# Kernel tuning notes

Hardware: AMD Instinct MI355X
Metric: run time of the kernel (lower is better)

## Reference

```python
import jax, jax.numpy as jnp
import numpy as np

T, B, IN, H = 256, 128, 512, 1024


def setup_inputs() -> dict:
    key = jax.random.key(0)
    ks = jax.random.split(key, 13)
    s = 1.0 / float(np.sqrt(H))  # torch LSTMCell init: U(-1/sqrt(H), 1/sqrt(H))
    u = lambda k, shp: jax.random.uniform(k, shp, jnp.float32, -s, s)
    return {
        "x": jax.random.normal(ks[0], (T, B, IN), jnp.float32),
        "h0_fwd": jax.random.normal(ks[1], (B, H), jnp.float32),
        "c0_fwd": jax.random.normal(ks[2], (B, H), jnp.float32),
        "h0_rev": jax.random.normal(ks[3], (B, H), jnp.float32),
        "c0_rev": jax.random.normal(ks[4], (B, H), jnp.float32),
        "W_ih_f": u(ks[5], (4 * H, IN)),
        "W_hh_f": u(ks[6], (4 * H, H)),
        "b_ih_f": u(ks[7], (4 * H,)),
        "b_hh_f": u(ks[8], (4 * H,)),
        "W_ih_r": u(ks[9], (4 * H, IN)),
        "W_hh_r": u(ks[10], (4 * H, H)),
        "b_ih_r": u(ks[11], (4 * H,)),
        "b_hh_r": u(ks[12], (4 * H,)),
    }


def _lstm(x, h0, c0, Wih, Whh, bih, bhh, reverse):
    # Precompute the input projection for all timesteps in one big GEMM.
    xp = jnp.einsum('tbi,gi->tbg', x, Wih) + bih + bhh  # [T, B, 4H]

    def step(carry, xg):
        h, c = carry
        gates = xg + h @ Whh.T  # [B, 4H]
        i, f, g, o = jnp.split(gates, 4, axis=-1)  # torch gate order: i, f, g, o
        c = jax.nn.sigmoid(f) * c + jax.nn.sigmoid(i) * jnp.tanh(g)
        h = jax.nn.sigmoid(o) * jnp.tanh(c)
        return (h, c), h

    # reverse=True scans backward in time but emits outputs in original order,
    # exactly matching ReverseLSTMLayer's reverse-process-then-reverse-outputs.
    (h, c), ys = jax.lax.scan(step, (h0, c0), xp, reverse=reverse)
    return ys, h, c


def reference(x, h0_fwd, c0_fwd, h0_rev, c0_rev,
              W_ih_f, W_hh_f, b_ih_f, b_hh_f,
              W_ih_r, W_hh_r, b_ih_r, b_hh_r):
    yf, hf, cf = _lstm(x, h0_fwd, c0_fwd, W_ih_f, W_hh_f, b_ih_f, b_hh_f, False)
    yr, hr, cr = _lstm(x, h0_rev, c0_rev, W_ih_r, W_hh_r, b_ih_r, b_hh_r, True)
    out = jnp.concatenate([yf, yr], axis=-1)  # [T, B, 2H]
    # Faithful to the original's `hidden, cell = output_states` quirk:
    # `hidden` is the forward direction's (h, c) pair stacked,
    # `cell` is the reverse direction's (h, c) pair stacked.
    hidden = jnp.stack([hf, cf])  # [2, B, H]
    cell = jnp.stack([hr, cr])    # [2, B, H]
    return out, (hidden, cell)
```

## Files before the change

### kernel.cpp

```cpp
#include <hip/hip_runtime.h>
#include <hip/hip_bf16.h>

typedef unsigned short u16;
typedef __attribute__((ext_vector_type(8))) short bf16x8;
typedef __attribute__((ext_vector_type(8))) u16   u16x8;
typedef __attribute__((ext_vector_type(4))) float f32x4;

#define T_STEPS 256
#define BATCH   128
#define INDIM   512
#define HDIM    1024
#define GDIM    4096
#define KTOT    1536

#define OFF_XBF   ((size_t)0)
#define XBF_BYTES ((size_t)T_STEPS * BATCH * INDIM * 2)
#define OFF_BM    (OFF_XBF + XBF_BYTES)
#define BM_BYTES  ((size_t)2 * GDIM * KTOT * 2)
#define OFF_BIAS  (OFF_BM + BM_BYTES)
#define BIAS_BYTES ((size_t)2 * GDIM * 4)
#define OFF_CNT   (OFF_BIAS + BIAS_BYTES)
#define OFF_ROLL  (OFF_CNT + 8192)
#define ROLL_BYTES ((size_t)(T_STEPS + 1) * 2 * BATCH * HDIM * 2)
#define WS_NEED   (OFF_ROLL + ROLL_BYTES)

__device__ __forceinline__ u16 f2b(float f) {
  __hip_bfloat16 h = __float2bfloat16(f);
  return *reinterpret_cast<u16*>(&h);
}

__device__ __forceinline__ void glds16(const void* g, void* l) {
  __builtin_amdgcn_global_load_lds(
      (const __attribute__((address_space(1))) unsigned int*)g,
      (__attribute__((address_space(3))) unsigned int*)l, 16, 0, 0);
}

__global__ void k_cast_x(const float* __restrict__ x, u16* __restrict__ xs) {
  int i = blockIdx.x * 256 + threadIdx.x;
  int t   = i >> 13;
  int r13 = i & 8191;
  int row = r13 >> 6;
  int c0  = (r13 & 63) * 8;
  int q = row >> 5, rloc = row & 31;
  int mi = rloc >> 4, ar = rloc & 15;
  int kq = c0 >> 7, kr = c0 & 127;
  int ks = kr >> 5, h4 = (kr & 31) >> 3;
  int lane = h4 * 16 + ar;
  const float* src = x + ((size_t)t * BATCH + row) * INDIM + c0;
  f32x4 a = *reinterpret_cast<const f32x4*>(src);
  f32x4 b = *reinterpret_cast<const f32x4*>(src + 4);
  u16x8 u;
  u[0] = f2b(a[0]); u[1] = f2b(a[1]); u[2] = f2b(a[2]); u[3] = f2b(a[3]);
  u[4] = f2b(b[0]); u[5] = f2b(b[1]); u[6] = f2b(b[2]); u[7] = f2b(b[3]);
  size_t dst = ((((((size_t)t * 4 + q) * 4 + kq) * 4 + ks) * 2 + mi) * 64 + lane) * 8;
  *reinterpret_cast<u16x8*>(xs + dst) = u;
}

__global__ void k_build_b(const float* __restrict__ Whh_f, const float* __restrict__ Wih_f,
                          const float* __restrict__ Whh_r, const float* __restrict__ Wih_r,
                          u16* __restrict__ Bm) {
  int blk = blockIdx.x;
  int dir = blk >> 5, jt = blk & 31;
  const float* Whh = dir ? Whh_r : Whh_f;
  const float* Wih = dir ? Wih_r : Wih_f;
  u16* dst = Bm + (size_t)blk * 128 * KTOT;
  for (int c = 0; c < 128; c++) {
    int G = (c >> 5) * HDIM + jt * 32 + (c & 31);
    for (int k = threadIdx.x; k < KTOT; k += 256) {
      float v = (k < HDIM) ? Whh[(size_t)G * HDIM + k] : Wih[(size_t)G * INDIM + (k - HDIM)];
      dst[c * KTOT + k] = f2b(v);
    }
  }
}

__global__ void k_init(const float* __restrict__ h0f, const float* __restrict__ h0r,
                       const float* __restrict__ bihf, const float* __restrict__ bhhf,
                       const float* __restrict__ bihr, const float* __restrict__ bhhr,
                       u16* __restrict__ hroll, float* __restrict__ bias,
                       unsigned* __restrict__ flags) {
  int i = blockIdx.x * 256 + threadIdx.x;
  if (i < 2 * BATCH * HDIM) {
    int dir = i / (BATCH * HDIM);
    int rem = i - dir * BATCH * HDIM;
    int r = rem / HDIM, c = rem - r * HDIM;
    const float* h0 = dir ? h0r : h0f;
    char* hb = (char*)hroll;
    *(u16*)(hb + ((size_t)dir * BATCH + r) * 2048 + ((2 * c) ^ ((r & 7) << 4))) =
        f2b(h0[rem]);
  }
  if (i < 2 * GDIM) {
    int dir = i / GDIM, g = i - dir * GDIM;
    bias[i] = dir ? (bihr[g] + bhhr[g]) : (bihf[g] + bhhf[g]);
  }
  if (i < 512) flags[i] = 0;
}

__global__ __launch_bounds__(512, 2) void k_lstm(
    const u16* __restrict__ xs, const u16* __restrict__ Bm,
    u16* __restrict__ hroll,
    const float* __restrict__ bias, unsigned* __restrict__ flags,
    const float* __restrict__ c0f, const float* __restrict__ c0r,
    float* __restrict__ out) {
  __shared__ float ldsf[34816];
  char* ldsc = reinterpret_cast<char*>(ldsf);
  float* ldsP = ldsf + 16384;

  __builtin_amdgcn_fence(__ATOMIC_ACQUIRE, "agent");

  const int wg   = blockIdx.x;
  const int grp  = wg & 7;
  const int dir  = grp >> 2, q = grp & 3;
  const int jt32 = wg >> 3;
  const int tid  = threadIdx.x;
  const int w = tid >> 6, lane = tid & 63;
  const int kq = w >> 1, nh = w & 1;
  const int h4 = lane >> 4, kk = h4 * 8;
  const int ar = lane & 15;

  const u16* bsrc = Bm + (size_t)(dir * 32 + jt32) * 128 * KTOT;
  bf16x8 bh[8][4], bx[4][4];
#pragma unroll
  for (int ks = 0; ks < 8; ks++)
#pragma unroll
    for (int ni = 0; ni < 4; ni++)
      bh[ks][ni] = *reinterpret_cast<const bf16x8*>(
          bsrc + (size_t)(nh * 64 + ni * 16 + ar) * KTOT + 256 * kq + 32 * ks + kk);
#pragma unroll
  for (int ks = 0; ks < 4; ks++)
#pragma unroll
    for (int ni = 0; ni < 4; ni++)
      bx[ks][ni] = *reinterpret_cast<const bf16x8*>(
          bsrc + (size_t)(nh * 64 + ni * 16 + ar) * KTOT + HDIM + 128 * kq + 32 * ks + kk);

  const int rrow = tid & 31;
  const int jl0  = 2 * (tid >> 5);
  const int row0 = q * 32 + rrow;
  const int jg0  = jt32 * 32 + jl0;
  const float* c0 = dir ? c0r : c0f;
  float2 cc = *reinterpret_cast<const float2*>(c0 + (size_t)row0 * HDIM + jg0);
  float cst0 = cc.x, cst1 = cc.y;
  const float2 b_i = *reinterpret_cast<const float2*>(bias + dir * GDIM + 0 * HDIM + jg0);
  const float2 b_f = *reinterpret_cast<const float2*>(bias + dir * GDIM + 1 * HDIM + jg0);
  const float2 b_g = *reinterpret_cast<const float2*>(bias + dir * GDIM + 2 * HDIM + jg0);
  const float2 b_o = *reinterpret_cast<const float2*>(bias + dir * GDIM + 3 * HDIM + jg0);

  const unsigned* fpA = flags + grp * 32 + (lane & 31);

#pragma unroll 1
  for (int s = 0; s < T_STEPS; s++) {
    const int t = dir ? (T_STEPS - 1 - s) : s;

    bf16x8 ax[4][2];
    {
      const u16* xb = xs + ((((size_t)t * 4 + q) * 4 + kq) * 4) * 2 * 512;
#pragma unroll
      for (int ks = 0; ks < 4; ks++)
#pragma unroll
        for (int mi = 0; mi < 2; mi++)
          ax[ks][mi] = *reinterpret_cast<const bf16x8*>(
              xb + ((size_t)(ks * 2 + mi) * 64 + lane) * 8);
    }

    if (s > 0) {
      while (true) {
        unsigned f = __hip_atomic_load(fpA, __ATOMIC_RELAXED, __HIP_MEMORY_SCOPE_AGENT);
        if (__all((int)(f >= (unsigned)s))) break;
        __builtin_amdgcn_s_sleep(1);
      }
      __builtin_amdgcn_sched_barrier(0);
    }

    {
      const char* hRd = (const char*)hroll + ((size_t)s * 2 + dir) * (BATCH * 2048)
                        + (size_t)q * 32 * 2048;
      unsigned off = (unsigned)tid * 16;
#pragma unroll
      for (int i = 0; i < 8; i++)
        glds16(hRd + off + i * 8192, ldsc + off + i * 8192);
    }
    __builtin_amdgcn_sched_barrier(0);

    f32x4 acc[2][4];
#pragma unroll
    for (int mi = 0; mi < 2; mi++)
#pragma unroll
      for (int ni = 0; ni < 4; ni++) acc[mi][ni] = f32x4{0.f, 0.f, 0.f, 0.f};
#pragma unroll
    for (int ks = 0; ks < 4; ks++)
#pragma unroll
      for (int mi = 0; mi < 2; mi++)
#pragma unroll
        for (int ni = 0; ni < 4; ni++)
          acc[mi][ni] = __builtin_amdgcn_mfma_f32_16x16x32_bf16(ax[ks][mi], bx[ks][ni], acc[mi][ni], 0, 0, 0);

    __syncthreads();

#pragma unroll
    for (int ks = 0; ks < 8; ks++) {
      bf16x8 af[2];
#pragma unroll
      for (int mi = 0; mi < 2; mi++) {
        unsigned row = 16 * mi + ar;
        unsigned cb = (256 * kq + 32 * ks + kk) * 2;
        af[mi] = *reinterpret_cast<const bf16x8*>(
            ldsc + row * 2048 + (cb ^ ((row & 7) << 4)));
      }
#pragma unroll
      for (int mi = 0; mi < 2; mi++)
#pragma unroll
        for (int ni = 0; ni < 4; ni++)
          acc[mi][ni] = __builtin_amdgcn_mfma_f32_16x16x32_bf16(af[mi], bh[ks][ni], acc[mi][ni], 0, 0, 0);
    }

    {
      float* pw = ldsP + kq * (128 * 36);
#pragma unroll
      for (int mi = 0; mi < 2; mi++)
#pragma unroll
        for (int ni = 0; ni < 4; ni++) {
          int col = nh * 64 + ni * 16 + ar;
          *reinterpret_cast<f32x4*>(pw + col * 36 + mi * 16 + h4 * 4) = acc[mi][ni];
        }
    }
    __syncthreads();

    float h0v, h1v;
    {
      float gi0 = b_i.x, gi1 = b_i.y, gf0 = b_f.x, gf1 = b_f.y;
      float gg0 = b_g.x, gg1 = b_g.y, go0 = b_o.x, go1 = b_o.y;
#pragma unroll
      for (int k4 = 0; k4 < 4; k4++) {
        const float* p = ldsP + k4 * (128 * 36);
        gi0 += p[(0 * 32 + jl0) * 36 + rrow]; gi1 += p[(0 * 32 + jl0 + 1) * 36 + rrow];
        gf0 += p[(1 * 32 + jl0) * 36 + rrow]; gf1 += p[(1 * 32 + jl0 + 1) * 36 + rrow];
        gg0 += p[(2 * 32 + jl0) * 36 + rrow]; gg1 += p[(2 * 32 + jl0 + 1) * 36 + rrow];
        go0 += p[(3 * 32 + jl0) * 36 + rrow]; go1 += p[(3 * 32 + jl0 + 1) * 36 + rrow];
      }
      float i0 = 1.f / (1.f + __expf(-gi0)), i1 = 1.f / (1.f + __expf(-gi1));
      float f0 = 1.f / (1.f + __expf(-gf0)), f1 = 1.f / (1.f + __expf(-gf1));
      float g0 = tanhf(gg0), g1 = tanhf(gg1);
      float o0 = 1.f / (1.f + __expf(-go0)), o1 = 1.f / (1.f + __expf(-go1));
      cst0 = f0 * cst0 + i0 * g0;
      cst1 = f1 * cst1 + i1 * g1;
      h0v = o0 * tanhf(cst0);
      h1v = o1 * tanhf(cst1);

      unsigned hp = (unsigned)f2b(h0v) | ((unsigned)f2b(h1v) << 16);
      char* hb = (char*)hroll + ((size_t)(s + 1) * 2 + dir) * (BATCH * 2048);
      __hip_atomic_store(
          (unsigned*)(hb + (size_t)row0 * 2048 + ((2 * jg0) ^ ((row0 & 7) << 4))),
          hp, __ATOMIC_RELAXED, __HIP_MEMORY_SCOPE_AGENT);
    }

    asm volatile("s_waitcnt vmcnt(0)" ::: "memory");
    __syncthreads();
    if (tid == 0)
      __hip_atomic_store(flags + grp * 32 + jt32, (unsigned)(s + 1),
                         __ATOMIC_RELAXED, __HIP_MEMORY_SCOPE_AGENT);

    {
      float2 yv; yv.x = h0v; yv.y = h1v;
      *reinterpret_cast<float2*>(out + ((size_t)t * BATCH + row0) * (2 * HDIM)
                                     + (size_t)dir * HDIM + jg0) = yv;
      if (s == T_STEPS - 1) {
        size_t hid = (size_t)T_STEPS * BATCH * 2 * HDIM;
        size_t base2 = hid + (size_t)dir * 2 * BATCH * HDIM;
        *reinterpret_cast<float2*>(out + base2 + (size_t)row0 * HDIM + jg0) = yv;
        float2 cv; cv.x = cst0; cv.y = cst1;
        *reinterpret_cast<float2*>(out + base2 + (size_t)BATCH * HDIM
                                       + (size_t)row0 * HDIM + jg0) = cv;
      }
    }
  }
}

extern "C" void kernel_launch(void* const* d_in, const int* in_sizes, int n_in,
                              void* d_out, int out_size, void* d_ws, size_t ws_size,
                              hipStream_t stream) {
  const float* x     = (const float*)d_in[0];
  const float* h0f   = (const float*)d_in[1];
  const float* c0f   = (const float*)d_in[2];
  const float* h0r   = (const float*)d_in[3];
  const float* c0r   = (const float*)d_in[4];
  const float* Wih_f = (const float*)d_in[5];
  const float* Whh_f = (const float*)d_in[6];
  const float* bih_f = (const float*)d_in[7];
  const float* bhh_f = (const float*)d_in[8];
  const float* Wih_r = (const float*)d_in[9];
  const float* Whh_r = (const float*)d_in[10];
  const float* bih_r = (const float*)d_in[11];
  const float* bhh_r = (const float*)d_in[12];
  float* out = (float*)d_out;
  char* ws = (char*)d_ws;

  if (ws_size < WS_NEED) return;

  u16* xsf        = (u16*)(ws + OFF_XBF);
  u16* Bm         = (u16*)(ws + OFF_BM);
  float* bias     = (float*)(ws + OFF_BIAS);
  unsigned* flags = (unsigned*)(ws + OFF_CNT);
  u16* hroll      = (u16*)(ws + OFF_ROLL);

  k_cast_x<<<8192, 256, 0, stream>>>(x, xsf);
  k_build_b<<<64, 256, 0, stream>>>(Whh_f, Wih_f, Whh_r, Wih_r, Bm);
  k_init<<<1024, 256, 0, stream>>>(h0f, h0r, bih_f, bhh_f, bih_r, bhh_r,
                                   hroll, bias, flags);
  k_lstm<<<256, 512, 0, stream>>>(xsf, Bm, hroll, bias, flags, c0f, c0r, out);
}
```

Before: 2.292 ms.

## Simplify x cast layout, reblock weights, alias LDS buffers, retune reduction padding

Several changes at once. The x cast becomes a plain row-major bf16 conversion and the LSTM kernel reads MFMA fragments directly with strided loads. The weight panel is rebuilt in 16-column blocks, and the LDS h buffer and partial-sum buffer now share one allocation, which needs an extra barrier. The partial-sum row pitch changes from 36 to 33, the gate thread mapping is swapped, and the h store scope drops to workgroup. The workgroup-scope store risks cross-workgroup visibility problems, and the strided x loads may be less coalesced.

```diff
diff --git a/kernel.cpp b/kernel.cpp
--- a/kernel.cpp
+++ b/kernel.cpp
@@ -35,37 +35,26 @@
       (__attribute__((address_space(3))) unsigned int*)l, 16, 0, 0);
 }
 
-__global__ void k_cast_x(const float* __restrict__ x, u16* __restrict__ xs) {
-  int i = blockIdx.x * 256 + threadIdx.x;
-  int t   = i >> 13;
-  int r13 = i & 8191;
-  int row = r13 >> 6;
-  int c0  = (r13 & 63) * 8;
-  int q = row >> 5, rloc = row & 31;
-  int mi = rloc >> 4, ar = rloc & 15;
-  int kq = c0 >> 7, kr = c0 & 127;
-  int ks = kr >> 5, h4 = (kr & 31) >> 3;
-  int lane = h4 * 16 + ar;
-  const float* src = x + ((size_t)t * BATCH + row) * INDIM + c0;
-  f32x4 a = *reinterpret_cast<const f32x4*>(src);
-  f32x4 b = *reinterpret_cast<const f32x4*>(src + 4);
+__global__ void k_cast_x(const float* __restrict__ x, u16* __restrict__ xb) {
+  size_t i = ((size_t)blockIdx.x * 256 + threadIdx.x) * 8;
+  f32x4 a = *reinterpret_cast<const f32x4*>(x + i);
+  f32x4 b = *reinterpret_cast<const f32x4*>(x + i + 4);
   u16x8 u;
   u[0] = f2b(a[0]); u[1] = f2b(a[1]); u[2] = f2b(a[2]); u[3] = f2b(a[3]);
   u[4] = f2b(b[0]); u[5] = f2b(b[1]); u[6] = f2b(b[2]); u[7] = f2b(b[3]);
-  size_t dst = ((((((size_t)t * 4 + q) * 4 + kq) * 4 + ks) * 2 + mi) * 64 + lane) * 8;
-  *reinterpret_cast<u16x8*>(xs + dst) = u;
+  *reinterpret_cast<u16x8*>(xb + i) = u;
 }
 
 __global__ void k_build_b(const float* __restrict__ Whh_f, const float* __restrict__ Wih_f,
                           const float* __restrict__ Whh_r, const float* __restrict__ Wih_r,
                           u16* __restrict__ Bm) {
   int blk = blockIdx.x;
-  int dir = blk >> 5, jt = blk & 31;
+  int dir = blk >> 6, jt = blk & 63;
   const float* Whh = dir ? Whh_r : Whh_f;
   const float* Wih = dir ? Wih_r : Wih_f;
-  u16* dst = Bm + (size_t)blk * 128 * KTOT;
-  for (int c = 0; c < 128; c++) {
-    int G = (c >> 5) * HDIM + jt * 32 + (c & 31);
+  u16* dst = Bm + (size_t)blk * 64 * KTOT;
+  for (int c = 0; c < 64; c++) {
+    int G = (c >> 4) * HDIM + jt * 16 + (c & 15);
     for (int k = threadIdx.x; k < KTOT; k += 256) {
       float v = (k < HDIM) ? Whh[(size_t)G * HDIM + k] : Wih[(size_t)G * INDIM + (k - HDIM)];
       dst[c * KTOT + k] = f2b(v);
@@ -96,44 +85,42 @@
 }
 
 __global__ __launch_bounds__(512, 2) void k_lstm(
-    const u16* __restrict__ xs, const u16* __restrict__ Bm,
+    const u16* __restrict__ xb, const u16* __restrict__ Bm,
     u16* __restrict__ hroll,
     const float* __restrict__ bias, unsigned* __restrict__ flags,
     const float* __restrict__ c0f, const float* __restrict__ c0r,
     float* __restrict__ out) {
-  __shared__ float ldsf[34816];
-  char* ldsc = reinterpret_cast<char*>(ldsf);
-  float* ldsP = ldsf + 16384;
+  __shared__ char ldsc[67584];
+  float* ldsP = reinterpret_cast<float*>(ldsc);
 
   __builtin_amdgcn_fence(__ATOMIC_ACQUIRE, "agent");
 
   const int wg   = blockIdx.x;
-  const int grp  = wg & 7;
-  const int dir  = grp >> 2, q = grp & 3;
+  const int xcd  = wg & 7;
+  const int dir  = xcd >> 2, q = xcd & 3;
   const int jt32 = wg >> 3;
+  const int grp  = dir * 4 + q;
   const int tid  = threadIdx.x;
   const int w = tid >> 6, lane = tid & 63;
   const int kq = w >> 1, nh = w & 1;
   const int h4 = lane >> 4, kk = h4 * 8;
   const int ar = lane & 15;
 
-  const u16* bsrc = Bm + (size_t)(dir * 32 + jt32) * 128 * KTOT;
   bf16x8 bh[8][4], bx[4][4];
 #pragma unroll
-  for (int ks = 0; ks < 8; ks++)
-#pragma unroll
-    for (int ni = 0; ni < 4; ni++)
-      bh[ks][ni] = *reinterpret_cast<const bf16x8*>(
-          bsrc + (size_t)(nh * 64 + ni * 16 + ar) * KTOT + 256 * kq + 32 * ks + kk);
-#pragma unroll
-  for (int ks = 0; ks < 4; ks++)
-#pragma unroll
-    for (int ni = 0; ni < 4; ni++)
-      bx[ks][ni] = *reinterpret_cast<const bf16x8*>(
-          bsrc + (size_t)(nh * 64 + ni * 16 + ar) * KTOT + HDIM + 128 * kq + 32 * ks + kk);
-
-  const int rrow = tid & 31;
-  const int jl0  = 2 * (tid >> 5);
+  for (int ni = 0; ni < 4; ni++) {
+    const u16* bp = Bm + (size_t)(dir * 64 + jt32 * 2 + (ni & 1)) * 64 * KTOT
+                  + (size_t)((nh * 2 + (ni >> 1)) * 16 + ar) * KTOT;
+#pragma unroll
+    for (int ks = 0; ks < 8; ks++)
+      bh[ks][ni] = *reinterpret_cast<const bf16x8*>(bp + 256 * kq + 32 * ks + kk);
+#pragma unroll
+    for (int ksx = 0; ksx < 4; ksx++)
+      bx[ksx][ni] = *reinterpret_cast<const bf16x8*>(bp + HDIM + 128 * kq + 32 * ksx + kk);
+  }
+
+  const int rrow = tid >> 4;
+  const int jl0  = 2 * (tid & 15);
   const int row0 = q * 32 + rrow;
   const int jg0  = jt32 * 32 + jl0;
   const float* c0 = dir ? c0r : c0f;
@@ -152,13 +139,13 @@
 
     bf16x8 ax[4][2];
     {
-      const u16* xb = xs + ((((size_t)t * 4 + q) * 4 + kq) * 4) * 2 * 512;
-#pragma unroll
-      for (int ks = 0; ks < 4; ks++)
+      const u16* xsrc = xb + ((size_t)t * BATCH + q * 32) * INDIM;
+#pragma unroll
+      for (int ksx = 0; ksx < 4; ksx++)
 #pragma unroll
         for (int mi = 0; mi < 2; mi++)
-          ax[ks][mi] = *reinterpret_cast<const bf16x8*>(
-              xb + ((size_t)(ks * 2 + mi) * 64 + lane) * 8);
+          ax[ksx][mi] = *reinterpret_cast<const bf16x8*>(
+              xsrc + (size_t)(16 * mi + ar) * INDIM + 128 * kq + 32 * ksx + kk);
     }
 
     if (s > 0) {
@@ -171,14 +158,13 @@
     }
 
     {
-      const char* hRd = (const char*)hroll + ((size_t)s * 2 + dir) * (BATCH * 2048)
-                        + (size_t)q * 32 * 2048;
+      const char* hRd = (const char*)hroll
+                      + ((size_t)(s * 2 + dir) * BATCH + q * 32) * 2048;
       unsigned off = (unsigned)tid * 16;
 #pragma unroll
       for (int i = 0; i < 8; i++)
         glds16(hRd + off + i * 8192, ldsc + off + i * 8192);
     }
-    __builtin_amdgcn_sched_barrier(0);
 
     f32x4 acc[2][4];
 #pragma unroll
@@ -186,12 +172,12 @@
 #pragma unroll
       for (int ni = 0; ni < 4; ni++) acc[mi][ni] = f32x4{0.f, 0.f, 0.f, 0.f};
 #pragma unroll
-    for (int ks = 0; ks < 4; ks++)
+    for (int ksx = 0; ksx < 4; ksx++)
 #pragma unroll
       for (int mi = 0; mi < 2; mi++)
 #pragma unroll
         for (int ni = 0; ni < 4; ni++)
-          acc[mi][ni] = __builtin_amdgcn_mfma_f32_16x16x32_bf16(ax[ks][mi], bx[ks][ni], acc[mi][ni], 0, 0, 0);
+          acc[mi][ni] = __builtin_amdgcn_mfma_f32_16x16x32_bf16(ax[ksx][mi], bx[ksx][ni], acc[mi][ni], 0, 0, 0);
 
     __syncthreads();
 
@@ -211,15 +197,16 @@
         for (int ni = 0; ni < 4; ni++)
           acc[mi][ni] = __builtin_amdgcn_mfma_f32_16x16x32_bf16(af[mi], bh[ks][ni], acc[mi][ni], 0, 0, 0);
     }
-
-    {
-      float* pw = ldsP + kq * (128 * 36);
+    __syncthreads();
+
+    {
+      float* pw = ldsP + kq * (128 * 33);
 #pragma unroll
       for (int mi = 0; mi < 2; mi++)
 #pragma unroll
         for (int ni = 0; ni < 4; ni++) {
           int col = nh * 64 + ni * 16 + ar;
-          *reinterpret_cast<f32x4*>(pw + col * 36 + mi * 16 + h4 * 4) = acc[mi][ni];
+          *reinterpret_cast<f32x4*>(pw + col * 33 + mi * 16 + h4 * 4) = acc[mi][ni];
         }
     }
     __syncthreads();
@@ -230,11 +217,11 @@
       float gg0 = b_g.x, gg1 = b_g.y, go0 = b_o.x, go1 = b_o.y;
 #pragma unroll
       for (int k4 = 0; k4 < 4; k4++) {
-        const float* p = ldsP + k4 * (128 * 36);
-        gi0 += p[(0 * 32 + jl0) * 36 + rrow]; gi1 += p[(0 * 32 + jl0 + 1) * 36 + rrow];
-        gf0 += p[(1 * 32 + jl0) * 36 + rrow]; gf1 += p[(1 * 32 + jl0 + 1) * 36 + rrow];
-        gg0 += p[(2 * 32 + jl0) * 36 + rrow]; gg1 += p[(2 * 32 + jl0 + 1) * 36 + rrow];
-        go0 += p[(3 * 32 + jl0) * 36 + rrow]; go1 += p[(3 * 32 + jl0 + 1) * 36 + rrow];
+        const float* p = ldsP + k4 * (128 * 33);
+        gi0 += p[(0 * 32 + jl0) * 33 + rrow]; gi1 += p[(0 * 32 + jl0 + 1) * 33 + rrow];
+        gf0 += p[(1 * 32 + jl0) * 33 + rrow]; gf1 += p[(1 * 32 + jl0 + 1) * 33 + rrow];
+        gg0 += p[(2 * 32 + jl0) * 33 + rrow]; gg1 += p[(2 * 32 + jl0 + 1) * 33 + rrow];
+        go0 += p[(3 * 32 + jl0) * 33 + rrow]; go1 += p[(3 * 32 + jl0 + 1) * 33 + rrow];
       }
       float i0 = 1.f / (1.f + __expf(-gi0)), i1 = 1.f / (1.f + __expf(-gi1));
       float f0 = 1.f / (1.f + __expf(-gf0)), f1 = 1.f / (1.f + __expf(-gf1));
@@ -246,10 +233,10 @@
       h1v = o1 * tanhf(cst1);
 
       unsigned hp = (unsigned)f2b(h0v) | ((unsigned)f2b(h1v) << 16);
-      char* hb = (char*)hroll + ((size_t)(s + 1) * 2 + dir) * (BATCH * 2048);
+      char* hb = (char*)hroll + ((size_t)((s + 1) * 2 + dir) * BATCH) * 2048;
       __hip_atomic_store(
           (unsigned*)(hb + (size_t)row0 * 2048 + ((2 * jg0) ^ ((row0 & 7) << 4))),
-          hp, __ATOMIC_RELAXED, __HIP_MEMORY_SCOPE_AGENT);
+          hp, __ATOMIC_RELAXED, __HIP_MEMORY_SCOPE_WORKGROUP);
     }
 
     asm volatile("s_waitcnt vmcnt(0)" ::: "memory");
@@ -295,15 +282,15 @@
 
   if (ws_size < WS_NEED) return;
 
-  u16* xsf        = (u16*)(ws + OFF_XBF);
+  u16* xbf        = (u16*)(ws + OFF_XBF);
   u16* Bm         = (u16*)(ws + OFF_BM);
   float* bias     = (float*)(ws + OFF_BIAS);
   unsigned* flags = (unsigned*)(ws + OFF_CNT);
   u16* hroll      = (u16*)(ws + OFF_ROLL);
 
-  k_cast_x<<<8192, 256, 0, stream>>>(x, xsf);
-  k_build_b<<<64, 256, 0, stream>>>(Whh_f, Wih_f, Whh_r, Wih_r, Bm);
+  k_cast_x<<<8192, 256, 0, stream>>>(x, xbf);
+  k_build_b<<<128, 256, 0, stream>>>(Whh_f, Wih_f, Whh_r, Wih_r, Bm);
   k_init<<<1024, 256, 0, stream>>>(h0f, h0r, bih_f, bhh_f, bih_r, bhh_r,
                                    hroll, bias, flags);
-  k_lstm<<<256, 512, 0, stream>>>(xsf, Bm, hroll, bias, flags, c0f, c0r, out);
-}
+  k_lstm<<<256, 512, 0, stream>>>(xbf, Bm, hroll, bias, flags, c0f, c0r, out);
+}
```

Measured after the change: 2.280 ms. Within noise of the previous version (-0.5%).
